# Performance work log

Hardware: AMD Instinct MI355X
Metric: run time of the kernel (lower is better)

The kernel has to match this reference:

```python
import jax, jax.numpy as jnp
import numpy as np

N, E, G, D, L = 100000, 1600000, 64, 128, 4
CLS_HID, NUM_CLASSES = 256, 10
BN_EPS = 1e-5


def setup_inputs() -> dict:
    key = jax.random.key(0)
    ks = jax.random.split(key, 16)
    s = 0.05
    cls_in = D + L * D  # sum(dims) = 640
    return {
        "node_deg": jax.random.randint(ks[0], (N,), 0, D),
        "edge_index": jax.random.randint(ks[1], (2, E), 0, N),
        "batch_vec": jnp.sort(jax.random.randint(ks[2], (N,), 0, G)),
        "eps": jnp.zeros((L,), jnp.float32),  # GINConv train_eps init 0
        "W1": jax.random.normal(ks[3], (L, D, D), jnp.float32) * s,
        "b1": jax.random.normal(ks[4], (L, D), jnp.float32) * s,
        "W2": jax.random.normal(ks[5], (L, D, D), jnp.float32) * s,
        "b2": jax.random.normal(ks[6], (L, D), jnp.float32) * s,
        "bn_g": jnp.ones((L, D), jnp.float32),
        "bn_b": jnp.zeros((L, D), jnp.float32),
        "Wc1": jax.random.normal(ks[7], (cls_in, CLS_HID), jnp.float32) * s,
        "bc1": jax.random.normal(ks[8], (CLS_HID,), jnp.float32) * s,
        "Wc2": jax.random.normal(ks[9], (CLS_HID, NUM_CLASSES), jnp.float32) * s,
        "bc2": jax.random.normal(ks[10], (NUM_CLASSES,), jnp.float32) * s,
    }


def reference(node_deg, edge_index, batch_vec, eps, W1, b1, W2, b2, bn_g, bn_b, Wc1, bc1, Wc2, bc2):
    n = node_deg.shape[0]
    src, dst = edge_index[0], edge_index[1]
    # OneHotEmbedding of node degree -> initial node features [N, D]
    x = jax.nn.one_hot(node_deg, D, dtype=jnp.float32)
    zs = [x]
    for l in range(eps.shape[0]):
        h_in = zs[-1]
        # GINConv: (1+eps)*x + scatter-add of neighbor features
        agg = jax.ops.segment_sum(h_in[src], dst, num_segments=n)
        h = (1.0 + eps[l]) * h_in + agg
        # mlp: lin -> lrelu -> lin
        h = jax.nn.leaky_relu(h @ W1[l] + b1[l])
        h = h @ W2[l] + b2[l]
        # BatchNorm1d over nodes (training-mode batch stats, biased var)
        mean = h.mean(axis=0)
        var = h.var(axis=0)
        h = (h - mean) * jax.lax.rsqrt(var + BN_EPS) * bn_g[l] + bn_b[l]
        zs.append(jax.nn.leaky_relu(h))
    z = jnp.concatenate(zs, axis=1)  # [N, 640]
    pooled = jax.ops.segment_sum(z, batch_vec, num_segments=G)  # global_add_pool
    pooled = jax.nn.leaky_relu(pooled)
    # classifier head: Linear -> LeakyReLU -> Linear (drop_out=0)
    h = jax.nn.leaky_relu(pooled @ Wc1 + bc1)
    return h @ Wc2 + bc2
```

## Files before the change

kernel.cpp:

```cpp
#include <hip/hip_runtime.h>
#include <hip/hip_bf16.h>


#define N_NODES   100000
#define N_EDGES   1600000
#define N_GRAPHS  64
#define DIM       128
#define N_LAYERS  4
#define CLS_IN    640
#define CLS_HID   256
#define N_CLASSES 10
#define LRELU_SLOPE 0.01f
#define BN_EPS_F    1e-5f

#define NBUCK    782
#define BUCK_CAP 4096

typedef __attribute__((ext_vector_type(8))) short bf16x8;
typedef __attribute__((ext_vector_type(4))) float f32x4;

__device__ __forceinline__ float lrelu(float x) { return x > 0.f ? x : LRELU_SLOPE * x; }

__device__ __forceinline__ ushort bf16r(float x) {
    uint a = __float_as_uint(x);
    return (ushort)((a + 0x7FFFu + ((a >> 16) & 1u)) >> 16);
}
__device__ __forceinline__ uint pack2(float x, float y) {
    uint a = __float_as_uint(x), b = __float_as_uint(y);
    a = (a + 0x7FFFu + ((a >> 16) & 1u)) >> 16;
    b = (b + 0x7FFFu + ((b >> 16) & 1u)) >> 16;
    return a | (b << 16);
}
__device__ __forceinline__ float2 unpack2(uint v) {
    return make_float2(__uint_as_float(v << 16), __uint_as_float(v & 0xFFFF0000u));
}

__global__ void k_convert_w(const float* __restrict__ W1, const float* __restrict__ W2,
                            ushort* __restrict__ W1t, ushort* __restrict__ W2t) {
    int gid = blockIdx.x * blockDim.x + threadIdx.x;
    if (gid >= 8 * DIM * DIM) return;
    int mat = gid >> 14, idx = gid & 16383;
    int k = idx >> 7, n = idx & 127;
    const float* src = (mat < 4) ? (W1 + mat * DIM * DIM) : (W2 + (mat - 4) * DIM * DIM);
    ushort* dst = (mat < 4) ? (W1t + mat * DIM * DIM) : (W2t + (mat - 4) * DIM * DIM);
    dst[n * DIM + k] = bf16r(src[k * DIM + n]);
}

__global__ void k_build_x(const int* __restrict__ deg, const int* __restrict__ batch,
                          uint* __restrict__ x, float* __restrict__ pooled) {
    int gid = blockIdx.x * blockDim.x + threadIdx.x;
    if (gid >= N_NODES * 64) return;
    int i = gid >> 6, c = gid & 63;
    int d = deg[i];
    uint v = 0;
    if ((d >> 1) == c) v = 0x3F80u << (16 * (d & 1));
    x[gid] = v;
    if (c == 0) atomicAdd(&pooled[batch[i] * CLS_IN + d], 1.0f);
}

__global__ void __launch_bounds__(1024) k_partition(const int* __restrict__ src,
                                                    const int* __restrict__ dst,
                                                    uint* __restrict__ cursor,
                                                    uint* __restrict__ ebuf) {
    __shared__ uint hist[NBUCK];
    __shared__ uint basev[NBUCK];
    int t = threadIdx.x;
    for (int b = t; b < NBUCK; b += 1024) hist[b] = 0;
    __syncthreads();
    int e0 = blockIdx.x * 16384;
    uint msrc[16], mdst[16], mrank[16];
#pragma unroll
    for (int i = 0; i < 16; ++i) {
        int e = e0 + i * 1024 + t;
        if (e < N_EDGES) {
            msrc[i] = (uint)src[e];
            mdst[i] = (uint)dst[e];
            mrank[i] = atomicAdd(&hist[mdst[i] >> 7], 1u);
        } else mdst[i] = 0xFFFFFFFFu;
    }
    __syncthreads();
    for (int b = t; b < NBUCK; b += 1024) {
        uint c = hist[b];
        basev[b] = c ? (uint)(b * BUCK_CAP) + atomicAdd(&cursor[b], c) : 0u;
    }
    __syncthreads();
#pragma unroll
    for (int i = 0; i < 16; ++i) {
        if (mdst[i] != 0xFFFFFFFFu) {
            uint b = mdst[i] >> 7;
            ebuf[basev[b] + mrank[i]] = ((mdst[i] & 127u) << 17) | msrc[i];
        }
    }
}

__global__ void __launch_bounds__(1024) k_bases(const uint* __restrict__ cursor,
                                                uint* __restrict__ base,
                                                int* __restrict__ indptr) {
    __shared__ uint sh[1024];
    int t = threadIdx.x;
    uint v = (t < NBUCK) ? min(cursor[t], (uint)BUCK_CAP) : 0u;
    sh[t] = v; __syncthreads();
    for (int off = 1; off < 1024; off <<= 1) {
        uint add = (t >= off) ? sh[t - off] : 0u;
        __syncthreads();
        sh[t] += add;
        __syncthreads();
    }
    if (t < NBUCK) base[t] = sh[t] - v;
    if (t == NBUCK - 1) indptr[N_NODES] = (int)sh[t];
}

__global__ void __launch_bounds__(512) k_sort(const uint* __restrict__ ebuf,
                                              const uint* __restrict__ cursor,
                                              const uint* __restrict__ base,
                                              int* __restrict__ csr,
                                              int* __restrict__ indptr) {
    __shared__ uint sortedL[BUCK_CAP];
    __shared__ uint hist[128];
    __shared__ uint startv[129];
    const int t = threadIdx.x, b = blockIdx.x;
    int cnt = (int)cursor[b]; if (cnt > BUCK_CAP) cnt = BUCK_CAP;
    if (t < 128) hist[t] = 0;
    __syncthreads();
    uint ent[8], rank[8];
    const uint* ep = ebuf + b * BUCK_CAP;
#pragma unroll
    for (int k = 0; k < 8; ++k) {
        int i = t + k * 512;
        if (i < cnt) { ent[k] = ep[i]; rank[k] = atomicAdd(&hist[ent[k] >> 17], 1u); }
    }
    __syncthreads();
    if (t < 128) startv[t + 1] = hist[t];
    if (t == 0) startv[0] = 0;
    __syncthreads();
    for (int off = 1; off < 128; off <<= 1) {
        uint add = (t < 128 && t >= off) ? startv[t + 1 - off] : 0u;
        __syncthreads();
        if (t < 128 && t >= off) startv[t + 1] += add;
        __syncthreads();
    }
#pragma unroll
    for (int k = 0; k < 8; ++k) {
        int i = t + k * 512;
        if (i < cnt) sortedL[startv[ent[k] >> 17] + rank[k]] = ent[k];
    }
    __syncthreads();
    int gbase = (int)base[b];
    for (int i = t; i < cnt; i += 512)
        csr[gbase + i] = (int)(sortedL[i] & 0x1FFFFu);
    if (t < 128) {
        int node = b * 128 + t;
        if (node < N_NODES) indptr[node] = gbase + (int)startv[t];
    }
}

__global__ void __launch_bounds__(512) k_agg4(const uint* __restrict__ h,
                                              const int* __restrict__ indptr,
                                              const int* __restrict__ csr,
                                              uint* __restrict__ out,
                                              const float* __restrict__ epsv, int layer) {
    __shared__ int eL[BUCK_CAP];
    __shared__ int sv[129];
    const int t = threadIdx.x, lane = t & 63, wave = t >> 6;
    const int b = blockIdx.x, node0 = b * 128;
    if (t < 129) {
        int node = node0 + t;
        sv[t] = indptr[node > N_NODES ? N_NODES : node];
    }
    __syncthreads();
    const int gbase = sv[0];
    const int cnt = sv[128] - gbase;
    for (int i = t; i < cnt; i += 512) eL[i] = csr[gbase + i];
    __syncthreads();
    const float s = 1.0f + epsv[layer];
    for (int ri = 0; ri < 16; ++ri) {
        int r = wave * 16 + ri;
        int g = node0 + r;
        if (g >= N_NODES) break;
        int beg = sv[r] - gbase, end = sv[r + 1] - gbase;
        float2 own = unpack2(h[g * 64 + lane]);
        float ax = s * own.x, ay = s * own.y;
        int j = beg;
        for (; j + 4 <= end; j += 4) {
            int i0 = eL[j], i1 = eL[j + 1], i2 = eL[j + 2], i3 = eL[j + 3];
            uint w0 = h[i0 * 64 + lane], w1 = h[i1 * 64 + lane];
            uint w2 = h[i2 * 64 + lane], w3 = h[i3 * 64 + lane];
            float2 f0 = unpack2(w0), f1 = unpack2(w1), f2 = unpack2(w2), f3 = unpack2(w3);
            ax += (f0.x + f1.x) + (f2.x + f3.x);
            ay += (f0.y + f1.y) + (f2.y + f3.y);
        }
        for (; j < end; ++j) {
            int u = eL[j];
            float2 f = unpack2(h[u * 64 + lane]);
            ax += f.x; ay += f.y;
        }
        out[g * 64 + lane] = pack2(ax, ay);
    }
}

#define MLP_LDS_BYTES 69632
__global__ void __launch_bounds__(256) k_mlp(const ushort* __restrict__ A,
                                             const ushort* __restrict__ W1t,
                                             const float* __restrict__ b1,
                                             const ushort* __restrict__ W2t,
                                             const float* __restrict__ b2,
                                             ushort* __restrict__ C,
                                             float* __restrict__ stats) {
    __shared__ char pool[MLP_LDS_BYTES];
    ushort* As = (ushort*)pool;
    ushort* Ws = (ushort*)(pool + 34816);
    float*  Cs = (float*)pool;
    const int t = threadIdx.x;
    const int row0 = blockIdx.x * 128;
    {
        int r = t >> 1, hh = t & 1;
        uint4* l = (uint4*)(As + r * 136 + hh * 64);
        if (row0 + r < N_NODES) {
            const uint4* g = (const uint4*)(A + (size_t)(row0 + r) * DIM + hh * 64);
#pragma unroll
            for (int k = 0; k < 8; ++k) l[k] = g[k];
        } else {
            uint4 z = make_uint4(0, 0, 0, 0);
#pragma unroll
            for (int k = 0; k < 8; ++k) l[k] = z;
        }
        const uint4* gw = (const uint4*)(W1t + r * DIM + hh * 64);
        uint4* lw = (uint4*)(Ws + r * 136 + hh * 64);
#pragma unroll
        for (int k = 0; k < 8; ++k) lw[k] = gw[k];
    }
    __syncthreads();
    const int lane = t & 63, wave = t >> 6;
    const int q = lane >> 4, m = lane & 15;
    const int R = (wave >> 1) * 64, Cb = (wave & 1) * 64;
    {
        f32x4 acc[4][4] = {};
#pragma unroll
        for (int ks = 0; ks < 4; ++ks) {
            bf16x8 a[4], b[4];
#pragma unroll
            for (int i = 0; i < 4; ++i)
                a[i] = *(const bf16x8*)(As + (R + i * 16 + m) * 136 + ks * 32 + q * 8);
#pragma unroll
            for (int j = 0; j < 4; ++j)
                b[j] = *(const bf16x8*)(Ws + (Cb + j * 16 + m) * 136 + ks * 32 + q * 8);
#pragma unroll
            for (int i = 0; i < 4; ++i)
#pragma unroll
                for (int j = 0; j < 4; ++j)
                    acc[i][j] = __builtin_amdgcn_mfma_f32_16x16x32_bf16(a[i], b[j], acc[i][j], 0, 0, 0);
        }
        __syncthreads();
        float bias1[4];
#pragma unroll
        for (int j = 0; j < 4; ++j) bias1[j] = b1[Cb + j * 16 + m];
#pragma unroll
        for (int i = 0; i < 4; ++i)
#pragma unroll
            for (int j = 0; j < 4; ++j)
#pragma unroll
                for (int r = 0; r < 4; ++r)
                    As[(R + i * 16 + q * 4 + r) * 136 + Cb + j * 16 + m] =
                        bf16r(lrelu(acc[i][j][r] + bias1[j]));
        {
            int r = t >> 1, hh = t & 1;
            const uint4* gw = (const uint4*)(W2t + r * DIM + hh * 64);
            uint4* lw = (uint4*)(Ws + r * 136 + hh * 64);
#pragma unroll
            for (int k = 0; k < 8; ++k) lw[k] = gw[k];
        }
    }
    __syncthreads();
    f32x4 acc2[4][4] = {};
#pragma unroll
    for (int ks = 0; ks < 4; ++ks) {
        bf16x8 a[4], b[4];
#pragma unroll
        for (int i = 0; i < 4; ++i)
            a[i] = *(const bf16x8*)(As + (R + i * 16 + m) * 136 + ks * 32 + q * 8);
#pragma unroll
        for (int j = 0; j < 4; ++j)
            b[j] = *(const bf16x8*)(Ws + (Cb + j * 16 + m) * 136 + ks * 32 + q * 8);
#pragma unroll
        for (int i = 0; i < 4; ++i)
#pragma unroll
            for (int j = 0; j < 4; ++j)
                acc2[i][j] = __builtin_amdgcn_mfma_f32_16x16x32_bf16(a[i], b[j], acc2[i][j], 0, 0, 0);
    }
    __syncthreads();
    float bias2[4];
#pragma unroll
    for (int j = 0; j < 4; ++j) bias2[j] = b2[Cb + j * 16 + m];
#pragma unroll
    for (int i = 0; i < 4; ++i)
#pragma unroll
        for (int j = 0; j < 4; ++j)
#pragma unroll
            for (int r = 0; r < 4; ++r)
                Cs[(R + i * 16 + q * 4 + r) * 132 + Cb + j * 16 + m] = acc2[i][j][r] + bias2[j];
    __syncthreads();
    if (t < DIM) {
        int rows = N_NODES - row0; if (rows > 128) rows = 128;
        float s1 = 0.f, s2 = 0.f;
        for (int r = 0; r < rows; ++r) { float v = Cs[r * 132 + t]; s1 += v; s2 += v * v; }
        atomicAdd(&stats[t], s1);
        atomicAdd(&stats[DIM + t], s2);
    }
    {
        int r = t >> 1, hh = t & 1;
        if (row0 + r < N_NODES) {
            uint4* outp = (uint4*)(C + (size_t)(row0 + r) * DIM + hh * 64);
#pragma unroll
            for (int k = 0; k < 8; ++k) {
                float4 v0 = *(const float4*)(Cs + r * 132 + hh * 64 + k * 8);
                float4 v1 = *(const float4*)(Cs + r * 132 + hh * 64 + k * 8 + 4);
                uint4 o;
                o.x = pack2(v0.x, v0.y); o.y = pack2(v0.z, v0.w);
                o.z = pack2(v1.x, v1.y); o.w = pack2(v1.z, v1.w);
                outp[k] = o;
            }
        }
    }
}

#define PROWS 128
__global__ void __launch_bounds__(256) k_bnpool(const uint* __restrict__ src,
                                                uint* __restrict__ dst,
                                                const float* __restrict__ stats,
                                                const float* __restrict__ bn_g,
                                                const float* __restrict__ bn_b, int layer,
                                                const int* __restrict__ batch,
                                                float* __restrict__ pooled, int colOff) {
    int c = threadIdx.x & 63;
    int chunk = threadIdx.x >> 6;
    int r0 = blockIdx.x * PROWS + chunk * (PROWS / 4);
    float sc0, sh0, sc1, sh1;
    {
        int f0 = 2 * c, f1 = 2 * c + 1;
        float m0 = stats[f0] * (1.0f / N_NODES);
        float m1 = stats[f1] * (1.0f / N_NODES);
        float v0 = stats[DIM + f0] * (1.0f / N_NODES) - m0 * m0;
        float v1 = stats[DIM + f1] * (1.0f / N_NODES) - m1 * m1;
        sc0 = bn_g[layer * DIM + f0] * rsqrtf(v0 + BN_EPS_F);
        sc1 = bn_g[layer * DIM + f1] * rsqrtf(v1 + BN_EPS_F);
        sh0 = bn_b[layer * DIM + f0] - m0 * sc0;
        sh1 = bn_b[layer * DIM + f1] - m1 * sc1;
    }
    int curg = -1;
    float a0 = 0.f, a1 = 0.f;
    for (int i = 0; i < PROWS / 4; ++i) {
        int r = r0 + i;
        if (r >= N_NODES) break;
        float2 v = unpack2(src[r * 64 + c]);
        float x0 = lrelu(v.x * sc0 + sh0);
        float x1 = lrelu(v.y * sc1 + sh1);
        dst[r * 64 + c] = pack2(x0, x1);
        int g = batch[r];
        if (g != curg) {
            if (curg >= 0) {
                atomicAdd(&pooled[curg * CLS_IN + colOff + 2 * c], a0);
                atomicAdd(&pooled[curg * CLS_IN + colOff + 2 * c + 1], a1);
            }
            curg = g; a0 = 0.f; a1 = 0.f;
        }
        a0 += x0; a1 += x1;
    }
    if (curg >= 0) {
        atomicAdd(&pooled[curg * CLS_IN + colOff + 2 * c], a0);
        atomicAdd(&pooled[curg * CLS_IN + colOff + 2 * c + 1], a1);
    }
}

__global__ void __launch_bounds__(256) k_classifier(const float* __restrict__ pooled,
                                                    const float* __restrict__ Wc1,
                                                    const float* __restrict__ bc1,
                                                    const float* __restrict__ Wc2,
                                                    const float* __restrict__ bc2,
                                                    float* __restrict__ out) {
    __shared__ float p[CLS_IN];
    __shared__ float hh[CLS_HID];
    int g = blockIdx.x, t = threadIdx.x;
    for (int j = t; j < CLS_IN; j += 256) p[j] = lrelu(pooled[g * CLS_IN + j]);
    __syncthreads();
    float acc = bc1[t];
    for (int k = 0; k < CLS_IN; ++k) acc += p[k] * Wc1[k * CLS_HID + t];
    hh[t] = lrelu(acc);
    __syncthreads();
    if (t < N_CLASSES) {
        float a2 = bc2[t];
        for (int k = 0; k < CLS_HID; ++k) a2 += hh[k] * Wc2[k * N_CLASSES + t];
        out[g * N_CLASSES + t] = a2;
    }
}

extern "C" void kernel_launch(void* const* d_in, const int* in_sizes, int n_in,
                              void* d_out, int out_size, void* d_ws, size_t ws_size,
                              hipStream_t stream) {
    const int*   deg   = (const int*)d_in[0];
    const int*   edges = (const int*)d_in[1];
    const int*   srcv  = edges;
    const int*   dstv  = edges + N_EDGES;
    const int*   batch = (const int*)d_in[2];
    const float* epsv  = (const float*)d_in[3];
    const float* W1    = (const float*)d_in[4];
    const float* b1    = (const float*)d_in[5];
    const float* W2    = (const float*)d_in[6];
    const float* b2    = (const float*)d_in[7];
    const float* bn_g  = (const float*)d_in[8];
    const float* bn_b  = (const float*)d_in[9];
    const float* Wc1   = (const float*)d_in[10];
    const float* bc1   = (const float*)d_in[11];
    const float* Wc2   = (const float*)d_in[12];
    const float* bc2   = (const float*)d_in[13];

    char* ws = (char*)d_ws;
    const size_t BUFB = (size_t)N_NODES * DIM * 2;
    size_t off = 0;
    ushort* buf0   = (ushort*)(ws + off); off += BUFB;
    ushort* buf1   = (ushort*)(ws + off); off += BUFB;
    ushort* W1t    = (ushort*)(ws + off); off += 4 * DIM * DIM * 2;
    ushort* W2t    = (ushort*)(ws + off); off += 4 * DIM * DIM * 2;
    float*  pooled = (float*)(ws + off);  off += N_GRAPHS * CLS_IN * 4;
    float*  statsA = (float*)(ws + off);  off += 4 * 2 * DIM * 4;
    uint*   cursor = (uint*)(ws + off);   off += (NBUCK + 8) * 4;
    uint*   base   = (uint*)(ws + off);   off += (NBUCK + 8) * 4;
    int*    indptr = (int*)(ws + off);    off += (N_NODES + 8) * 4;
    int*    csr    = (int*)(ws + off);    off += (size_t)N_EDGES * 4;
    uint*   ebuf   = (uint*)(ws + off);   off += (size_t)NBUCK * BUCK_CAP * 4;

    hipMemsetAsync(pooled, 0, N_GRAPHS * CLS_IN * 4, stream);
    hipMemsetAsync(statsA, 0, 4 * 2 * DIM * 4, stream);
    hipMemsetAsync(cursor, 0, NBUCK * 4, stream);

    k_convert_w<<<(8 * DIM * DIM + 255) / 256, 256, 0, stream>>>(W1, W2, W1t, W2t);
    k_build_x<<<(N_NODES * 64 + 255) / 256, 256, 0, stream>>>(deg, batch, (uint*)buf0, pooled);
    k_partition<<<(N_EDGES + 16383) / 16384, 1024, 0, stream>>>(srcv, dstv, cursor, ebuf);
    k_bases<<<1, 1024, 0, stream>>>(cursor, base, indptr);
    k_sort<<<NBUCK, 512, 0, stream>>>(ebuf, cursor, base, csr, indptr);

    const int gemm_grid = (N_NODES + 127) / 128;
    for (int l = 0; l < N_LAYERS; ++l) {
        float* stats = statsA + l * 2 * DIM;
        k_agg4<<<NBUCK, 512, 0, stream>>>((const uint*)buf0, indptr, csr,
                                          (uint*)buf1, epsv, l);
        k_mlp<<<gemm_grid, 256, 0, stream>>>(buf1, W1t + l * DIM * DIM, b1 + l * DIM,
                                             W2t + l * DIM * DIM, b2 + l * DIM,
                                             buf1, stats);
        k_bnpool<<<(N_NODES + PROWS - 1) / PROWS, 256, 0, stream>>>(
            (const uint*)buf1, (uint*)buf0, stats, bn_g, bn_b, l, batch,
            pooled, DIM * (l + 1));
    }

    k_classifier<<<N_GRAPHS, 256, 0, stream>>>(pooled, Wc1, bc1, Wc2, bc2, (float*)d_out);
}
```

Baseline: 675.9 us.

## Fuse neighbor aggregation into MLP kernel with 64-node tiles

Merges the sparse aggregation kernel and the two-layer MLP GEMM kernel into one per-layer kernel. Each block aggregates 64 nodes straight into shared memory and then runs both MFMA GEMMs, so the aggregated features no longer make a round trip through global memory and one launch per layer goes away. The tile is halved to 64 rows, with an edge-staging cap and a global-memory fallback for high-degree tiles. The pooling kernel's row tile is halved to match. Risks are lower MFMA work per block, W1/W2 reloaded twice as often, and more stats atomics from the larger grid.

```diff
diff --git a/kernel.cpp b/kernel.cpp
--- a/kernel.cpp
+++ b/kernel.cpp
@@ -15,6 +15,7 @@
 
 #define NBUCK    782
 #define BUCK_CAP 4096
+#define ECAP     1536
 
 typedef __attribute__((ext_vector_type(8))) short bf16x8;
 typedef __attribute__((ext_vector_type(4))) float f32x4;
@@ -154,98 +155,92 @@
     }
 }
 
-__global__ void __launch_bounds__(512) k_agg4(const uint* __restrict__ h,
-                                              const int* __restrict__ indptr,
-                                              const int* __restrict__ csr,
-                                              uint* __restrict__ out,
-                                              const float* __restrict__ epsv, int layer) {
-    __shared__ int eL[BUCK_CAP];
-    __shared__ int sv[129];
+#define LYR_LDS (17408 + 34816 + ECAP * 4 + 272)
+__global__ void __launch_bounds__(256) k_layer(const uint* __restrict__ h,
+                                               const int* __restrict__ indptr,
+                                               const int* __restrict__ csr,
+                                               const ushort* __restrict__ W1t,
+                                               const float* __restrict__ b1,
+                                               const ushort* __restrict__ W2t,
+                                               const float* __restrict__ b2,
+                                               ushort* __restrict__ C,
+                                               float* __restrict__ stats,
+                                               const float* __restrict__ epsv, int layer) {
+    __shared__ char pool[LYR_LDS];
+    ushort* As = (ushort*)pool;
+    ushort* Ws = (ushort*)(pool + 17408);
+    float*  Cs = (float*)(pool + 17408);
+    int*    eL = (int*)(pool + 17408 + 34816);
+    int*    sv = (int*)(pool + 17408 + 34816 + ECAP * 4);
     const int t = threadIdx.x, lane = t & 63, wave = t >> 6;
-    const int b = blockIdx.x, node0 = b * 128;
-    if (t < 129) {
-        int node = node0 + t;
-        sv[t] = indptr[node > N_NODES ? N_NODES : node];
+    const int node0 = blockIdx.x * 64;
+    if (t < 65) {
+        int n = node0 + t;
+        sv[t] = indptr[n > N_NODES ? N_NODES : n];
+    }
+    {
+        int rw = t >> 1, hh = t & 1;
+        const uint4* gw = (const uint4*)(W1t + rw * DIM + hh * 64);
+        uint4* lw = (uint4*)(Ws + rw * 136 + hh * 64);
+#pragma unroll
+        for (int k = 0; k < 8; ++k) lw[k] = gw[k];
     }
     __syncthreads();
     const int gbase = sv[0];
-    const int cnt = sv[128] - gbase;
-    for (int i = t; i < cnt; i += 512) eL[i] = csr[gbase + i];
+    {
+        int cnt = sv[64] - gbase;
+        int stg = cnt > ECAP ? ECAP : cnt;
+        for (int i = t; i < stg; i += 256) eL[i] = csr[gbase + i];
+    }
     __syncthreads();
     const float s = 1.0f + epsv[layer];
     for (int ri = 0; ri < 16; ++ri) {
         int r = wave * 16 + ri;
         int g = node0 + r;
-        if (g >= N_NODES) break;
+        uint* Arow = (uint*)(As + r * 136);
+        if (g >= N_NODES) { Arow[lane] = 0u; continue; }
         int beg = sv[r] - gbase, end = sv[r + 1] - gbase;
         float2 own = unpack2(h[g * 64 + lane]);
         float ax = s * own.x, ay = s * own.y;
-        int j = beg;
-        for (; j + 4 <= end; j += 4) {
-            int i0 = eL[j], i1 = eL[j + 1], i2 = eL[j + 2], i3 = eL[j + 3];
-            uint w0 = h[i0 * 64 + lane], w1 = h[i1 * 64 + lane];
-            uint w2 = h[i2 * 64 + lane], w3 = h[i3 * 64 + lane];
-            float2 f0 = unpack2(w0), f1 = unpack2(w1), f2 = unpack2(w2), f3 = unpack2(w3);
-            ax += (f0.x + f1.x) + (f2.x + f3.x);
-            ay += (f0.y + f1.y) + (f2.y + f3.y);
-        }
-        for (; j < end; ++j) {
-            int u = eL[j];
-            float2 f = unpack2(h[u * 64 + lane]);
-            ax += f.x; ay += f.y;
-        }
-        out[g * 64 + lane] = pack2(ax, ay);
-    }
-}
-
-#define MLP_LDS_BYTES 69632
-__global__ void __launch_bounds__(256) k_mlp(const ushort* __restrict__ A,
-                                             const ushort* __restrict__ W1t,
-                                             const float* __restrict__ b1,
-                                             const ushort* __restrict__ W2t,
-                                             const float* __restrict__ b2,
-                                             ushort* __restrict__ C,
-                                             float* __restrict__ stats) {
-    __shared__ char pool[MLP_LDS_BYTES];
-    ushort* As = (ushort*)pool;
-    ushort* Ws = (ushort*)(pool + 34816);
-    float*  Cs = (float*)pool;
-    const int t = threadIdx.x;
-    const int row0 = blockIdx.x * 128;
+        if (end <= ECAP) {
+            int j = beg;
+            for (; j + 4 <= end; j += 4) {
+                int i0 = eL[j], i1 = eL[j + 1], i2 = eL[j + 2], i3 = eL[j + 3];
+                uint w0 = h[i0 * 64 + lane], w1 = h[i1 * 64 + lane];
+                uint w2 = h[i2 * 64 + lane], w3 = h[i3 * 64 + lane];
+                float2 f0 = unpack2(w0), f1 = unpack2(w1), f2 = unpack2(w2), f3 = unpack2(w3);
+                ax += (f0.x + f1.x) + (f2.x + f3.x);
+                ay += (f0.y + f1.y) + (f2.y + f3.y);
+            }
+            for (; j < end; ++j) {
+                float2 f = unpack2(h[eL[j] * 64 + lane]);
+                ax += f.x; ay += f.y;
+            }
+        } else {
+            for (int j = beg; j < end; ++j) {
+                int u = csr[gbase + j];
+                float2 f = unpack2(h[u * 64 + lane]);
+                ax += f.x; ay += f.y;
+            }
+        }
+        Arow[lane] = pack2(ax, ay);
+    }
+    __syncthreads();
+    const int q = lane >> 4, m = lane & 15;
+    const int R = (wave >> 1) * 32, Cb = (wave & 1) * 64;
     {
-        int r = t >> 1, hh = t & 1;
-        uint4* l = (uint4*)(As + r * 136 + hh * 64);
-        if (row0 + r < N_NODES) {
-            const uint4* g = (const uint4*)(A + (size_t)(row0 + r) * DIM + hh * 64);
-#pragma unroll
-            for (int k = 0; k < 8; ++k) l[k] = g[k];
-        } else {
-            uint4 z = make_uint4(0, 0, 0, 0);
-#pragma unroll
-            for (int k = 0; k < 8; ++k) l[k] = z;
-        }
-        const uint4* gw = (const uint4*)(W1t + r * DIM + hh * 64);
-        uint4* lw = (uint4*)(Ws + r * 136 + hh * 64);
-#pragma unroll
-        for (int k = 0; k < 8; ++k) lw[k] = gw[k];
-    }
-    __syncthreads();
-    const int lane = t & 63, wave = t >> 6;
-    const int q = lane >> 4, m = lane & 15;
-    const int R = (wave >> 1) * 64, Cb = (wave & 1) * 64;
-    {
-        f32x4 acc[4][4] = {};
+        f32x4 acc[2][4] = {};
 #pragma unroll
         for (int ks = 0; ks < 4; ++ks) {
-            bf16x8 a[4], b[4];
-#pragma unroll
-            for (int i = 0; i < 4; ++i)
+            bf16x8 a[2], b[4];
+#pragma unroll
+            for (int i = 0; i < 2; ++i)
                 a[i] = *(const bf16x8*)(As + (R + i * 16 + m) * 136 + ks * 32 + q * 8);
 #pragma unroll
             for (int j = 0; j < 4; ++j)
                 b[j] = *(const bf16x8*)(Ws + (Cb + j * 16 + m) * 136 + ks * 32 + q * 8);
 #pragma unroll
-            for (int i = 0; i < 4; ++i)
+            for (int i = 0; i < 2; ++i)
 #pragma unroll
                 for (int j = 0; j < 4; ++j)
                     acc[i][j] = __builtin_amdgcn_mfma_f32_16x16x32_bf16(a[i], b[j], acc[i][j], 0, 0, 0);
@@ -255,7 +250,7 @@
 #pragma unroll
         for (int j = 0; j < 4; ++j) bias1[j] = b1[Cb + j * 16 + m];
 #pragma unroll
-        for (int i = 0; i < 4; ++i)
+        for (int i = 0; i < 2; ++i)
 #pragma unroll
             for (int j = 0; j < 4; ++j)
 #pragma unroll
@@ -263,26 +258,26 @@
                     As[(R + i * 16 + q * 4 + r) * 136 + Cb + j * 16 + m] =
                         bf16r(lrelu(acc[i][j][r] + bias1[j]));
         {
-            int r = t >> 1, hh = t & 1;
-            const uint4* gw = (const uint4*)(W2t + r * DIM + hh * 64);
-            uint4* lw = (uint4*)(Ws + r * 136 + hh * 64);
+            int rw = t >> 1, hh = t & 1;
+            const uint4* gw = (const uint4*)(W2t + rw * DIM + hh * 64);
+            uint4* lw = (uint4*)(Ws + rw * 136 + hh * 64);
 #pragma unroll
             for (int k = 0; k < 8; ++k) lw[k] = gw[k];
         }
     }
     __syncthreads();
-    f32x4 acc2[4][4] = {};
+    f32x4 acc2[2][4] = {};
 #pragma unroll
     for (int ks = 0; ks < 4; ++ks) {
-        bf16x8 a[4], b[4];
-#pragma unroll
-        for (int i = 0; i < 4; ++i)
+        bf16x8 a[2], b[4];
+#pragma unroll
+        for (int i = 0; i < 2; ++i)
             a[i] = *(const bf16x8*)(As + (R + i * 16 + m) * 136 + ks * 32 + q * 8);
 #pragma unroll
         for (int j = 0; j < 4; ++j)
             b[j] = *(const bf16x8*)(Ws + (Cb + j * 16 + m) * 136 + ks * 32 + q * 8);
 #pragma unroll
-        for (int i = 0; i < 4; ++i)
+        for (int i = 0; i < 2; ++i)
 #pragma unroll
             for (int j = 0; j < 4; ++j)
                 acc2[i][j] = __builtin_amdgcn_mfma_f32_16x16x32_bf16(a[i], b[j], acc2[i][j], 0, 0, 0);
@@ -292,7 +287,7 @@
 #pragma unroll
     for (int j = 0; j < 4; ++j) bias2[j] = b2[Cb + j * 16 + m];
 #pragma unroll
-    for (int i = 0; i < 4; ++i)
+    for (int i = 0; i < 2; ++i)
 #pragma unroll
         for (int j = 0; j < 4; ++j)
 #pragma unroll
@@ -300,30 +295,31 @@
                 Cs[(R + i * 16 + q * 4 + r) * 132 + Cb + j * 16 + m] = acc2[i][j][r] + bias2[j];
     __syncthreads();
     if (t < DIM) {
-        int rows = N_NODES - row0; if (rows > 128) rows = 128;
+        int rows = N_NODES - node0; if (rows > 64) rows = 64;
         float s1 = 0.f, s2 = 0.f;
         for (int r = 0; r < rows; ++r) { float v = Cs[r * 132 + t]; s1 += v; s2 += v * v; }
         atomicAdd(&stats[t], s1);
         atomicAdd(&stats[DIM + t], s2);
     }
     {
-        int r = t >> 1, hh = t & 1;
-        if (row0 + r < N_NODES) {
-            uint4* outp = (uint4*)(C + (size_t)(row0 + r) * DIM + hh * 64);
-#pragma unroll
-            for (int k = 0; k < 8; ++k) {
-                float4 v0 = *(const float4*)(Cs + r * 132 + hh * 64 + k * 8);
-                float4 v1 = *(const float4*)(Cs + r * 132 + hh * 64 + k * 8 + 4);
+        int r2 = t >> 2, c4 = t & 3;
+        if (node0 + r2 < N_NODES) {
+            uint4* outp = (uint4*)(C + (size_t)(node0 + r2) * DIM);
+#pragma unroll
+            for (int k = 0; k < 4; ++k) {
+                int chunk = c4 * 4 + k;
+                float4 v0 = *(const float4*)(Cs + r2 * 132 + chunk * 8);
+                float4 v1 = *(const float4*)(Cs + r2 * 132 + chunk * 8 + 4);
                 uint4 o;
                 o.x = pack2(v0.x, v0.y); o.y = pack2(v0.z, v0.w);
                 o.z = pack2(v1.x, v1.y); o.w = pack2(v1.z, v1.w);
-                outp[k] = o;
+                outp[chunk] = o;
             }
         }
     }
 }
 
-#define PROWS 128
+#define PROWS 64
 __global__ void __launch_bounds__(256) k_bnpool(const uint* __restrict__ src,
                                                 uint* __restrict__ dst,
                                                 const float* __restrict__ stats,
@@ -438,14 +434,13 @@
     k_bases<<<1, 1024, 0, stream>>>(cursor, base, indptr);
     k_sort<<<NBUCK, 512, 0, stream>>>(ebuf, cursor, base, csr, indptr);
 
-    const int gemm_grid = (N_NODES + 127) / 128;
+    const int layer_grid = (N_NODES + 63) / 64;
     for (int l = 0; l < N_LAYERS; ++l) {
         float* stats = statsA + l * 2 * DIM;
-        k_agg4<<<NBUCK, 512, 0, stream>>>((const uint*)buf0, indptr, csr,
-                                          (uint*)buf1, epsv, l);
-        k_mlp<<<gemm_grid, 256, 0, stream>>>(buf1, W1t + l * DIM * DIM, b1 + l * DIM,
-                                             W2t + l * DIM * DIM, b2 + l * DIM,
-                                             buf1, stats);
+        k_layer<<<layer_grid, 256, 0, stream>>>((const uint*)buf0, indptr, csr,
+                                                W1t + l * DIM * DIM, b1 + l * DIM,
+                                                W2t + l * DIM * DIM, b2 + l * DIM,
+                                                buf1, stats, epsv, l);
         k_bnpool<<<(N_NODES + PROWS - 1) / PROWS, 256, 0, stream>>>(
             (const uint*)buf1, (uint*)buf0, stats, bn_g, bn_b, l, batch,
             pooled, DIM * (l + 1));
```

New measurement: 1.032 ms. 1.53x slower.
